# Kernel optimization log

Hardware: AMD Instinct MI355X
Metric: run time of the kernel (lower is better)

## Reference

```python
import jax, jax.numpy as jnp
import numpy as np

D_MODEL = 1024
N_HEADS = 16
HEAD_DIM = D_MODEL // N_HEADS
EPS = 1e-6


def setup_inputs() -> dict:
    key = jax.random.key(0)
    ks = jax.random.split(key, 5)
    b, s = 2, 2048
    x = jax.random.normal(ks[0], (b, s, D_MODEL), dtype=jnp.float32)
    scale = 1.0 / np.sqrt(D_MODEL)
    Wq = jax.random.normal(ks[1], (D_MODEL, D_MODEL), dtype=jnp.float32) * scale
    Wk = jax.random.normal(ks[2], (D_MODEL, D_MODEL), dtype=jnp.float32) * scale
    Wv = jax.random.normal(ks[3], (D_MODEL, D_MODEL), dtype=jnp.float32) * scale
    Wo = jax.random.normal(ks[4], (D_MODEL, D_MODEL), dtype=jnp.float32) * scale
    return {"x": x, "Wq": Wq, "Wk": Wk, "Wv": Wv, "Wo": Wo}


def _feature_map(t):
    return jax.nn.relu(t) + EPS


def reference(x, Wq, Wk, Wv, Wo):
    b, s, _ = x.shape
    # nn.Linear applies x @ W.T
    q = (x @ Wq.T).reshape(b, s, N_HEADS, HEAD_DIM)
    k = (x @ Wk.T).reshape(b, s, N_HEADS, HEAD_DIM)
    v = (x @ Wv.T).reshape(b, s, N_HEADS, HEAD_DIM)
    q = _feature_map(q).transpose(0, 2, 1, 3)  # bhsd
    k = _feature_map(k).transpose(0, 2, 1, 3)  # bhsd
    v = v.transpose(0, 2, 1, 3)                # bhsm
    # cumulative KV outer products: (b,h,s,d,m)
    kv = jnp.einsum('bhsd,bhsm->bhsdm', k, v)
    kv_cum = jnp.cumsum(kv, axis=2)
    out = jnp.einsum('bhsd,bhsdm->bhsm', q, kv_cum)
    k_cum = jnp.cumsum(k, axis=2)
    z = 1.0 / (jnp.einsum('bhsd,bhsd->bhs', q, k_cum) + EPS)
    out = out * z[..., None]
    out = out.transpose(0, 2, 1, 3).reshape(b, s, D_MODEL)
    return out @ Wo.T
```

## Files before the change

### kernel.cpp

```cpp
#include <hip/hip_runtime.h>

#define EPSF 1e-6f

typedef short bf16x8_t __attribute__((ext_vector_type(8)));
typedef float f32x4_t __attribute__((ext_vector_type(4)));

__device__ __forceinline__ ushort f2bf(float f) {
  union { float f; uint32_t u; } c; c.f = f;
  return (ushort)((c.u + 0x7FFFu + ((c.u >> 16) & 1u)) >> 16);
}
__device__ __forceinline__ float bf2f(ushort u) {
  union { uint32_t u; float f; } c; c.u = ((uint32_t)u) << 16;
  return c.f;
}

#define SWB(row, kbyte) (((row) << 7) + ((kbyte) ^ (((row) & 7) << 4)))

__global__ __launch_bounds__(256) void cvt5_kernel(
    const float4* __restrict__ x, const float4* __restrict__ wq,
    const float4* __restrict__ wk, const float4* __restrict__ wv,
    const float4* __restrict__ wo,
    ushort4* __restrict__ xb, ushort4* __restrict__ wqb,
    ushort4* __restrict__ wkb, ushort4* __restrict__ wvb,
    ushort4* __restrict__ wob)
{
  const int i = blockIdx.x * 256 + threadIdx.x;
  const float4* src; ushort4* dst; int off;
  if (i < (1 << 20)) { src = x; dst = xb; off = i; }
  else {
    const int j = i - (1 << 20);
    const int r = j >> 18;
    off = j & ((1 << 18) - 1);
    src = (r == 0) ? wq : (r == 1) ? wk : (r == 2) ? wv : wo;
    dst = (r == 0) ? wqb : (r == 1) ? wkb : (r == 2) ? wvb : wob;
  }
  const float4 v = src[off];
  ushort4 o;
  o.x = f2bf(v.x); o.y = f2bf(v.y); o.z = f2bf(v.z); o.w = f2bf(v.w);
  dst[off] = o;
}

template<int RELU, int OUT_BF16>
__device__ __forceinline__ void gemm_bt_mfma(
    const ushort* __restrict__ A, const ushort* __restrict__ B,
    void* __restrict__ C, const int K, const int N,
    const int row0, const int col0)
{
  __shared__ __align__(16) ushort As[128 * 32];
  __shared__ __align__(16) ushort Bs[128 * 32];
  const int tid = threadIdx.x;
  const int lane = tid & 63;
  const int wv = tid >> 6;
  const int wr = (wv >> 1) * 64;
  const int wc = (wv & 1) * 64;

  f32x4_t acc[4][4];
#pragma unroll
  for (int m = 0; m < 4; ++m)
#pragma unroll
    for (int n = 0; n < 4; ++n) acc[m][n] = (f32x4_t){0.f, 0.f, 0.f, 0.f};

  const int fr = lane & 15;
  const int kh = (lane >> 4) * 8;

  for (int k0 = 0; k0 < K; k0 += 32) {
    __syncthreads();
#pragma unroll
    for (int issue = 0; issue < 2; ++issue) {
      const int chunk = wv * 64 + lane + issue * 256;
      const int row = chunk >> 2;
      const int kp = chunk & 3;
      const ushort* gsrcA = A + (size_t)(row0 + row) * K + k0 + kp * 8;
      const ushort* gsrcB = B + (size_t)(col0 + row) * K + k0 + kp * 8;
      ushort* ldstA = As + (size_t)(wv * 64 + issue * 256) * 8;
      ushort* ldstB = Bs + (size_t)(wv * 64 + issue * 256) * 8;
      __builtin_amdgcn_global_load_lds(
          (const __attribute__((address_space(1))) void*)gsrcA,
          (__attribute__((address_space(3))) void*)ldstA, 16, 0, 0);
      __builtin_amdgcn_global_load_lds(
          (const __attribute__((address_space(1))) void*)gsrcB,
          (__attribute__((address_space(3))) void*)ldstB, 16, 0, 0);
    }
    __syncthreads();

    bf16x8_t af[4], bfr[4];
#pragma unroll
    for (int m = 0; m < 4; ++m)
      af[m] = *(const bf16x8_t*)&As[(size_t)(wr + m * 16 + fr) * 32 + kh];
#pragma unroll
    for (int n = 0; n < 4; ++n)
      bfr[n] = *(const bf16x8_t*)&Bs[(size_t)(wc + n * 16 + fr) * 32 + kh];
#pragma unroll
    for (int m = 0; m < 4; ++m)
#pragma unroll
      for (int n = 0; n < 4; ++n)
        acc[m][n] = __builtin_amdgcn_mfma_f32_16x16x32_bf16(
            af[m], bfr[n], acc[m][n], 0, 0, 0);
  }

  const int rq = (lane >> 4) * 4;
#pragma unroll
  for (int m = 0; m < 4; ++m) {
#pragma unroll
    for (int r = 0; r < 4; ++r) {
      const size_t grow = (size_t)(row0 + wr + m * 16 + rq + r);
#pragma unroll
      for (int n = 0; n < 4; ++n) {
        float val = acc[m][n][r];
        if (RELU) val = fmaxf(val, 0.f) + EPSF;
        const size_t gcol = (size_t)(col0 + wc + n * 16 + fr);
        if (OUT_BF16) ((ushort*)C)[grow * N + gcol] = f2bf(val);
        else          ((float*)C)[grow * N + gcol] = val;
      }
    }
  }
}

__global__ __launch_bounds__(256) void qkv_gemm_kernel(
    const ushort* __restrict__ xb,
    const ushort* __restrict__ wqb, const ushort* __restrict__ wkb,
    const ushort* __restrict__ wvb,
    ushort* __restrict__ q, ushort* __restrict__ k, ushort* __restrict__ v)
{
  const int which = blockIdx.y >> 3;
  const int bcol = blockIdx.y & 7;
  const ushort* B = (which == 0) ? wqb : (which == 1) ? wkb : wvb;
  ushort* C = (which == 0) ? q : (which == 1) ? k : v;
  if (which < 2)
    gemm_bt_mfma<1, 1>(xb, B, C, 1024, 1024, blockIdx.x * 128, bcol * 128);
  else
    gemm_bt_mfma<0, 1>(xb, B, C, 1024, 1024, blockIdx.x * 128, bcol * 128);
}

__global__ __launch_bounds__(256) void out_gemm_kernel(
    const ushort* __restrict__ at, const ushort* __restrict__ wob,
    float* __restrict__ out)
{
  gemm_bt_mfma<0, 0>(at, wob, out, 1024, 1024, blockIdx.x * 128, blockIdx.y * 128);
}


__global__ __launch_bounds__(256) void chunk_sums_kernel(
    const ushort* __restrict__ kbuf, const ushort* __restrict__ vbuf,
    float* __restrict__ kvsum, float* __restrict__ ksum)
{
  __shared__ __align__(16) ushort Kt[64 * 64];
  __shared__ __align__(16) ushort Vt[64 * 64];
  const int chunk = blockIdx.x;
  const int seq = blockIdx.y;
  const int b = seq >> 4, h = seq & 15;
  const int tid = threadIdx.x;
  const size_t base = ((size_t)b * 2048 + chunk * 64) * 1024 + h * 64;

#pragma unroll
  for (int r = 0; r < 2; ++r) {
    const int idx = tid + (r << 8);
    const int j = idx >> 3;
    const int e0 = (idx & 7) << 3;
    const bf16x8_t kv8 = *(const bf16x8_t*)(kbuf + base + (size_t)j * 1024 + e0);
    const bf16x8_t vv8 = *(const bf16x8_t*)(vbuf + base + (size_t)j * 1024 + e0);
#pragma unroll
    for (int t = 0; t < 8; ++t) {
      *(ushort*)((char*)Kt + SWB(e0 + t, j * 2)) = (ushort)kv8[t];
      *(ushort*)((char*)Vt + SWB(e0 + t, j * 2)) = (ushort)vv8[t];
    }
  }
  __syncthreads();

  if (tid < 64) {
    float s = 0.f;
#pragma unroll
    for (int g = 0; g < 8; ++g) {
      const bf16x8_t kr = *(const bf16x8_t*)((char*)Kt + SWB(tid, g * 16));
#pragma unroll
      for (int t = 0; t < 8; ++t) s += bf2f((ushort)kr[t]);
    }
    ksum[((size_t)seq * 32 + chunk) * 64 + tid] = s;
  }

  const int lane = tid & 63;
  const int wv = tid >> 6;
  const int wm = (wv >> 1) * 32;
  const int wd = (wv & 1) * 32;
  const int fr = lane & 15;
  const int khb = (lane >> 4) * 16;

  f32x4_t acc[2][2];
#pragma unroll
  for (int m = 0; m < 2; ++m)
#pragma unroll
    for (int n = 0; n < 2; ++n) acc[m][n] = (f32x4_t){0.f, 0.f, 0.f, 0.f};

#pragma unroll
  for (int kk = 0; kk < 2; ++kk) {
    bf16x8_t av[2], bk[2];
#pragma unroll
    for (int m = 0; m < 2; ++m)
      av[m] = *(const bf16x8_t*)((char*)Vt + SWB(wm + m * 16 + fr, kk * 64 + khb));
#pragma unroll
    for (int n = 0; n < 2; ++n)
      bk[n] = *(const bf16x8_t*)((char*)Kt + SWB(wd + n * 16 + fr, kk * 64 + khb));
#pragma unroll
    for (int m = 0; m < 2; ++m)
#pragma unroll
      for (int n = 0; n < 2; ++n)
        acc[m][n] = __builtin_amdgcn_mfma_f32_16x16x32_bf16(
            av[m], bk[n], acc[m][n], 0, 0, 0);
  }

  const size_t kvbase = ((size_t)seq * 32 + chunk) << 12;
  const int rq = (lane >> 4) * 4;
#pragma unroll
  for (int m = 0; m < 2; ++m)
#pragma unroll
    for (int r = 0; r < 4; ++r) {
      const int mrow = wm + m * 16 + rq + r;
#pragma unroll
      for (int n = 0; n < 2; ++n) {
        const int dcol = wd + n * 16 + fr;
        kvsum[kvbase + (size_t)mrow * 64 + dcol] = acc[m][n][r];
      }
    }
}

__global__ __launch_bounds__(256) void scan_kernel(
    float* __restrict__ kvsum, float* __restrict__ ksum)
{
  const int slice = blockIdx.x & 15;
  const int seq = blockIdx.x >> 4;
  const int e = slice * 256 + threadIdx.x;
  const size_t base = ((size_t)seq << 17) + e;
  float run = 0.f;
  for (int c = 0; c < 32; ++c) {
    const size_t idx = base + ((size_t)c << 12);
    const float t = kvsum[idx];
    kvsum[idx] = run;
    run += t;
  }
  if (slice == 0 && threadIdx.x < 64) {
    const size_t kb = (size_t)seq * 2048 + threadIdx.x;
    float run2 = 0.f;
    for (int c = 0; c < 32; ++c) {
      const float t = ksum[kb + (size_t)c * 64];
      ksum[kb + (size_t)c * 64] = run2;
      run2 += t;
    }
  }
}

__global__ __launch_bounds__(256) void attn_chunk_kernel(
    const ushort* __restrict__ qbuf, const ushort* __restrict__ kbuf,
    const ushort* __restrict__ vbuf, const float* __restrict__ kvsum,
    const float* __restrict__ ksum, ushort* __restrict__ attn)
{
  __shared__ __align__(16) ushort Qs[64 * 64];
  __shared__ __align__(16) ushort Ks[64 * 64];
  __shared__ __align__(16) ushort Vt[64 * 64];
  __shared__ __align__(16) ushort Pl[64 * 64];
  __shared__ float ksp[64];
  __shared__ float zinv[64];
  const int chunk = blockIdx.x;
  const int seq = blockIdx.y;
  const int b = seq >> 4, h = seq & 15;
  const int tid = threadIdx.x;
  const size_t base = ((size_t)b * 2048 + chunk * 64) * 1024 + h * 64;

#pragma unroll
  for (int r = 0; r < 2; ++r) {
    const int idx = tid + (r << 8);
    const int row = idx >> 3;
    const int e0 = (idx & 7) << 3;
    const int kb = e0 << 1;
    *(bf16x8_t*)((char*)Qs + SWB(row, kb)) =
        *(const bf16x8_t*)(qbuf + base + (size_t)row * 1024 + e0);
    *(bf16x8_t*)((char*)Ks + SWB(row, kb)) =
        *(const bf16x8_t*)(kbuf + base + (size_t)row * 1024 + e0);
    const bf16x8_t vv8 = *(const bf16x8_t*)(vbuf + base + (size_t)row * 1024 + e0);
#pragma unroll
    for (int t = 0; t < 8; ++t)
      *(ushort*)((char*)Vt + SWB(e0 + t, row * 2)) = (ushort)vv8[t];
  }
  if (tid < 64) ksp[tid] = ksum[((size_t)seq * 32 + chunk) * 64 + tid];
  __syncthreads();

  const int lane = tid & 63;
  const int wv = tid >> 6;
  const int wr = (wv >> 1) * 32;
  const int wc = (wv & 1) * 32;
  const int fr = lane & 15;
  const int khb = (lane >> 4) * 16;
  const int rq = (lane >> 4) * 4;

  f32x4_t sf[2][2];
#pragma unroll
  for (int m = 0; m < 2; ++m)
#pragma unroll
    for (int n = 0; n < 2; ++n) sf[m][n] = (f32x4_t){0.f, 0.f, 0.f, 0.f};
#pragma unroll
  for (int kk = 0; kk < 2; ++kk) {
    bf16x8_t aq[2], bk[2];
#pragma unroll
    for (int m = 0; m < 2; ++m)
      aq[m] = *(const bf16x8_t*)((char*)Qs + SWB(wr + m * 16 + fr, kk * 64 + khb));
#pragma unroll
    for (int n = 0; n < 2; ++n)
      bk[n] = *(const bf16x8_t*)((char*)Ks + SWB(wc + n * 16 + fr, kk * 64 + khb));
#pragma unroll
    for (int m = 0; m < 2; ++m)
#pragma unroll
      for (int n = 0; n < 2; ++n)
        sf[m][n] = __builtin_amdgcn_mfma_f32_16x16x32_bf16(
            aq[m], bk[n], sf[m][n], 0, 0, 0);
  }
  __syncthreads();

#pragma unroll
  for (int m = 0; m < 2; ++m)
#pragma unroll
    for (int r = 0; r < 4; ++r) {
      const int i = wr + m * 16 + rq + r;
#pragma unroll
      for (int n = 0; n < 2; ++n) {
        const int j = wc + n * 16 + fr;
        const float pv = (j <= i) ? sf[m][n][r] : 0.f;
        *(ushort*)((char*)Pl + SWB(i, j * 2)) = f2bf(pv);
      }
    }
  const size_t kvbase = ((size_t)seq * 32 + chunk) << 12;
#pragma unroll
  for (int r = 0; r < 2; ++r) {
    const int idx = tid + (r << 8);
    const int mrow = idx >> 3;
    const int d0 = (idx & 7) << 3;
    const float4 lo = *(const float4*)(kvsum + kvbase + (size_t)mrow * 64 + d0);
    const float4 hi = *(const float4*)(kvsum + kvbase + (size_t)mrow * 64 + d0 + 4);
    bf16x8_t kv8;
    kv8[0] = (short)f2bf(lo.x); kv8[1] = (short)f2bf(lo.y);
    kv8[2] = (short)f2bf(lo.z); kv8[3] = (short)f2bf(lo.w);
    kv8[4] = (short)f2bf(hi.x); kv8[5] = (short)f2bf(hi.y);
    kv8[6] = (short)f2bf(hi.z); kv8[7] = (short)f2bf(hi.w);
    *(bf16x8_t*)((char*)Ks + SWB(mrow, d0 << 1)) = kv8;
  }
  __syncthreads();

  if (tid < 64) {
    const int i = tid;
    float dsum = 0.f, ssum = 0.f;
#pragma unroll
    for (int g = 0; g < 8; ++g) {
      const bf16x8_t qr = *(const bf16x8_t*)((char*)Qs + SWB(i, g * 16));
      const bf16x8_t pr = *(const bf16x8_t*)((char*)Pl + SWB(i, g * 16));
#pragma unroll
      for (int t = 0; t < 8; ++t) {
        dsum = fmaf(bf2f((ushort)qr[t]), ksp[g * 8 + t], dsum);
        ssum += bf2f((ushort)pr[t]);
      }
    }
    zinv[i] = 1.f / (dsum + ssum + EPSF);
  }

  f32x4_t of[2][2];
#pragma unroll
  for (int m = 0; m < 2; ++m)
#pragma unroll
    for (int n = 0; n < 2; ++n) of[m][n] = (f32x4_t){0.f, 0.f, 0.f, 0.f};
#pragma unroll
  for (int kk = 0; kk < 2; ++kk) {
    bf16x8_t ap[2], bv[2];
#pragma unroll
    for (int m = 0; m < 2; ++m)
      ap[m] = *(const bf16x8_t*)((char*)Pl + SWB(wr + m * 16 + fr, kk * 64 + khb));
#pragma unroll
    for (int n = 0; n < 2; ++n)
      bv[n] = *(const bf16x8_t*)((char*)Vt + SWB(wc + n * 16 + fr, kk * 64 + khb));
#pragma unroll
    for (int m = 0; m < 2; ++m)
#pragma unroll
      for (int n = 0; n < 2; ++n)
        of[m][n] = __builtin_amdgcn_mfma_f32_16x16x32_bf16(
            ap[m], bv[n], of[m][n], 0, 0, 0);
  }
#pragma unroll
  for (int kk = 0; kk < 2; ++kk) {
    bf16x8_t aq[2], bkv[2];
#pragma unroll
    for (int m = 0; m < 2; ++m)
      aq[m] = *(const bf16x8_t*)((char*)Qs + SWB(wr + m * 16 + fr, kk * 64 + khb));
#pragma unroll
    for (int n = 0; n < 2; ++n)
      bkv[n] = *(const bf16x8_t*)((char*)Ks + SWB(wc + n * 16 + fr, kk * 64 + khb));
#pragma unroll
    for (int m = 0; m < 2; ++m)
#pragma unroll
      for (int n = 0; n < 2; ++n)
        of[m][n] = __builtin_amdgcn_mfma_f32_16x16x32_bf16(
            aq[m], bkv[n], of[m][n], 0, 0, 0);
  }
  __syncthreads();

#pragma unroll
  for (int m = 0; m < 2; ++m)
#pragma unroll
    for (int r = 0; r < 4; ++r) {
      const int i = wr + m * 16 + rq + r;
      const float z = zinv[i];
#pragma unroll
      for (int n = 0; n < 2; ++n) {
        const int mcol = wc + n * 16 + fr;
        attn[base + (size_t)i * 1024 + mcol] = f2bf(of[m][n][r] * z);
      }
    }
}

extern "C" void kernel_launch(void* const* d_in, const int* in_sizes, int n_in,
                              void* d_out, int out_size, void* d_ws, size_t ws_size,
                              hipStream_t stream)
{
  (void)in_sizes; (void)n_in; (void)out_size; (void)ws_size;
  const float* x  = (const float*)d_in[0];
  const float* Wq = (const float*)d_in[1];
  const float* Wk = (const float*)d_in[2];
  const float* Wv = (const float*)d_in[3];
  const float* Wo = (const float*)d_in[4];
  float* out = (float*)d_out;

  const size_t NM = (size_t)4096 * 1024;
  ushort* xb  = (ushort*)d_ws;
  ushort* wqb = xb + NM;
  ushort* wkb = wqb + (1 << 20);
  ushort* wvb = wkb + (1 << 20);
  ushort* wob = wvb + (1 << 20);
  ushort* qb  = wob + (1 << 20);
  ushort* kb  = qb + NM;
  ushort* vb  = kb + NM;
  ushort* at  = vb + NM;
  float*  ksm = (float*)(at + NM);
  float*  kvs = (float*)d_out;

  cvt5_kernel<<<8192, 256, 0, stream>>>(
      (const float4*)x, (const float4*)Wq, (const float4*)Wk,
      (const float4*)Wv, (const float4*)Wo,
      (ushort4*)xb, (ushort4*)wqb, (ushort4*)wkb, (ushort4*)wvb, (ushort4*)wob);
  qkv_gemm_kernel<<<dim3(32, 24), 256, 0, stream>>>(xb, wqb, wkb, wvb, qb, kb, vb);
  chunk_sums_kernel<<<dim3(32, 32), 256, 0, stream>>>(kb, vb, kvs, ksm);
  scan_kernel<<<512, 256, 0, stream>>>(kvs, ksm);
  attn_chunk_kernel<<<dim3(32, 32), 256, 0, stream>>>(qb, kb, vb, kvs, ksm, at);
  out_gemm_kernel<<<dim3(32, 8), 256, 0, stream>>>(at, wob, out);
}
```

Baseline: 168.0 us.

## Double-buffer GEMM LDS tiles and batch loads in scan kernel

The bf16 MFMA GEMM now keeps two LDS buffers, so it can prefetch the next K-tile with global_load_lds while MFMAs run on the current one. It also raises wave priority around the MFMA block. The prefix-scan kernel now loads all 32 chunk values into registers before the scan loop, so the loads are not serialized behind the dependent stores. This doubles GEMM LDS usage, which could reduce occupancy, and the loop assumes K is a multiple of 64.

```diff
diff --git a/kernel.cpp b/kernel.cpp
--- a/kernel.cpp
+++ b/kernel.cpp
@@ -46,8 +46,8 @@
     void* __restrict__ C, const int K, const int N,
     const int row0, const int col0)
 {
-  __shared__ __align__(16) ushort As[128 * 32];
-  __shared__ __align__(16) ushort Bs[128 * 32];
+  __shared__ __align__(16) ushort As[2][128 * 32];
+  __shared__ __align__(16) ushort Bs[2][128 * 32];
   const int tid = threadIdx.x;
   const int lane = tid & 63;
   const int wv = tid >> 6;
@@ -63,40 +63,70 @@
   const int fr = lane & 15;
   const int kh = (lane >> 4) * 8;
 
-  for (int k0 = 0; k0 < K; k0 += 32) {
+  const int chunk0 = wv * 64 + lane;
+  const int chunk1 = chunk0 + 256;
+  const int rowA0 = chunk0 >> 2, kpA0 = (chunk0 & 3) << 3;
+  const int rowA1 = chunk1 >> 2, kpA1 = (chunk1 & 3) << 3;
+  const int ldoff0 = (wv * 64) * 8;
+  const int ldoff1 = (wv * 64 + 256) * 8;
+
+#define STAGE(buf, k0)                                                        \
+  do {                                                                        \
+    __builtin_amdgcn_global_load_lds(                                         \
+        (const __attribute__((address_space(1))) void*)(A +                   \
+            (size_t)(row0 + rowA0) * K + (k0) + kpA0),                        \
+        (__attribute__((address_space(3))) void*)(&As[buf][ldoff0]), 16, 0, 0);\
+    __builtin_amdgcn_global_load_lds(                                         \
+        (const __attribute__((address_space(1))) void*)(B +                   \
+            (size_t)(col0 + rowA0) * K + (k0) + kpA0),                        \
+        (__attribute__((address_space(3))) void*)(&Bs[buf][ldoff0]), 16, 0, 0);\
+    __builtin_amdgcn_global_load_lds(                                         \
+        (const __attribute__((address_space(1))) void*)(A +                   \
+            (size_t)(row0 + rowA1) * K + (k0) + kpA1),                        \
+        (__attribute__((address_space(3))) void*)(&As[buf][ldoff1]), 16, 0, 0);\
+    __builtin_amdgcn_global_load_lds(                                         \
+        (const __attribute__((address_space(1))) void*)(B +                   \
+            (size_t)(col0 + rowA1) * K + (k0) + kpA1),                        \
+        (__attribute__((address_space(3))) void*)(&Bs[buf][ldoff1]), 16, 0, 0);\
+  } while (0)
+
+#define COMPUTE(buf)                                                          \
+  do {                                                                        \
+    bf16x8_t af[4], bfr[4];                                                   \
+    _Pragma("unroll")                                                         \
+    for (int m = 0; m < 4; ++m)                                               \
+      af[m] = *(const bf16x8_t*)&As[buf][(wr + m * 16 + fr) * 32 + kh];       \
+    _Pragma("unroll")                                                         \
+    for (int n = 0; n < 4; ++n)                                               \
+      bfr[n] = *(const bf16x8_t*)&Bs[buf][(wc + n * 16 + fr) * 32 + kh];      \
+    __builtin_amdgcn_s_setprio(1);                                            \
+    _Pragma("unroll")                                                         \
+    for (int m = 0; m < 4; ++m)                                               \
+      _Pragma("unroll")                                                       \
+      for (int n = 0; n < 4; ++n)                                             \
+        acc[m][n] = __builtin_amdgcn_mfma_f32_16x16x32_bf16(                  \
+            af[m], bfr[n], acc[m][n], 0, 0, 0);                               \
+    __builtin_amdgcn_s_setprio(0);                                            \
+  } while (0)
+
+  const int NT = K >> 5;
+  STAGE(0, 0);
+  __syncthreads();
+  for (int t = 0; t < NT - 2; t += 2) {
+    STAGE(1, (t + 1) << 5);
+    COMPUTE(0);
     __syncthreads();
-#pragma unroll
-    for (int issue = 0; issue < 2; ++issue) {
-      const int chunk = wv * 64 + lane + issue * 256;
-      const int row = chunk >> 2;
-      const int kp = chunk & 3;
-      const ushort* gsrcA = A + (size_t)(row0 + row) * K + k0 + kp * 8;
-      const ushort* gsrcB = B + (size_t)(col0 + row) * K + k0 + kp * 8;
-      ushort* ldstA = As + (size_t)(wv * 64 + issue * 256) * 8;
-      ushort* ldstB = Bs + (size_t)(wv * 64 + issue * 256) * 8;
-      __builtin_amdgcn_global_load_lds(
-          (const __attribute__((address_space(1))) void*)gsrcA,
-          (__attribute__((address_space(3))) void*)ldstA, 16, 0, 0);
-      __builtin_amdgcn_global_load_lds(
-          (const __attribute__((address_space(1))) void*)gsrcB,
-          (__attribute__((address_space(3))) void*)ldstB, 16, 0, 0);
-    }
+    STAGE(0, (t + 2) << 5);
+    COMPUTE(1);
     __syncthreads();
-
-    bf16x8_t af[4], bfr[4];
-#pragma unroll
-    for (int m = 0; m < 4; ++m)
-      af[m] = *(const bf16x8_t*)&As[(size_t)(wr + m * 16 + fr) * 32 + kh];
-#pragma unroll
-    for (int n = 0; n < 4; ++n)
-      bfr[n] = *(const bf16x8_t*)&Bs[(size_t)(wc + n * 16 + fr) * 32 + kh];
-#pragma unroll
-    for (int m = 0; m < 4; ++m)
-#pragma unroll
-      for (int n = 0; n < 4; ++n)
-        acc[m][n] = __builtin_amdgcn_mfma_f32_16x16x32_bf16(
-            af[m], bfr[n], acc[m][n], 0, 0, 0);
-  }
+  }
+  STAGE(1, (NT - 1) << 5);
+  COMPUTE(0);
+  __syncthreads();
+  COMPUTE(1);
+
+#undef STAGE
+#undef COMPUTE
 
   const int rq = (lane >> 4) * 4;
 #pragma unroll
@@ -230,18 +260,25 @@
   const int seq = blockIdx.x >> 4;
   const int e = slice * 256 + threadIdx.x;
   const size_t base = ((size_t)seq << 17) + e;
+  float vals[32];
+#pragma unroll
+  for (int c = 0; c < 32; ++c) vals[c] = kvsum[base + ((size_t)c << 12)];
   float run = 0.f;
+#pragma unroll
   for (int c = 0; c < 32; ++c) {
-    const size_t idx = base + ((size_t)c << 12);
-    const float t = kvsum[idx];
-    kvsum[idx] = run;
+    const float t = vals[c];
+    kvsum[base + ((size_t)c << 12)] = run;
     run += t;
   }
   if (slice == 0 && threadIdx.x < 64) {
     const size_t kb = (size_t)seq * 2048 + threadIdx.x;
+    float kv2[32];
+#pragma unroll
+    for (int c = 0; c < 32; ++c) kv2[c] = ksum[kb + (size_t)c * 64];
     float run2 = 0.f;
+#pragma unroll
     for (int c = 0; c < 32; ++c) {
-      const float t = ksum[kb + (size_t)c * 64];
+      const float t = kv2[c];
       ksum[kb + (size_t)c * 64] = run2;
       run2 += t;
     }
```

After: 180.7 us. +7.5%, slower.
